# Kernel tuning notes

Measured on AMD Instinct MI355X. Metric: run time of the kernel, lower is better.

Reference implementation:

```python
import jax, jax.numpy as jnp
import numpy as np

N = 100000      # nodes
E = 1600000     # edges (avg degree 16)
F_IN = 64       # num_features
HID = 16        # hidden channels (fixed in module)
OUT = 32        # num_classes
K = 2           # kernel_size (dim=1, degree=1 open B-spline -> 2 basis fns)


def setup_inputs() -> dict:
    key = jax.random.key(0)
    ks = jax.random.split(key, 8)
    return {
        "x": jax.random.normal(ks[0], (N, F_IN), jnp.float32),
        "edge_index": jax.random.randint(ks[1], (2, E), 0, N, dtype=jnp.int64),
        "dropout": 0,  # unused in eval mode (F.dropout training=False)
        "edge_attr": jnp.full((E, 1), 0.1, jnp.float32),  # nt([0.1]) broadcast per edge
        "W1": jax.random.normal(ks[2], (K, F_IN, HID), jnp.float32) / np.sqrt(K * F_IN).astype(np.float32),
        "root1": jax.random.normal(ks[3], (F_IN, HID), jnp.float32) / np.sqrt(F_IN).astype(np.float32),
        "bias1": jnp.zeros((HID,), jnp.float32),
        "W2": jax.random.normal(ks[4], (K, HID, OUT), jnp.float32) / np.sqrt(K * HID).astype(np.float32),
        "root2": jax.random.normal(ks[5], (HID, OUT), jnp.float32) / np.sqrt(HID).astype(np.float32),
        "bias2": jnp.zeros((OUT,), jnp.float32),
    }


def spline_conv(x, edge_index, edge_attr, W, root, bias):
    """SplineConv, dim=1, kernel_size=2, degree=1 open B-spline, aggr='mean'."""
    src, dst = edge_index[0], edge_index[1]
    n = x.shape[0]
    u = edge_attr[:, 0]                                  # [E] pseudo-coords in [0,1]
    # degree-1 open spline, kernel_size=2: frac = u*(ks-1) = u; kernels {0,1}
    basis = jnp.stack([1.0 - u, u], axis=1)              # [E, K]
    # transform at node level (cheaper than gathering raw features per edge)
    h = jnp.einsum('nf,kfo->nko', x, W)                  # [N, K, out]
    msg = jnp.einsum('ek,eko->eo', basis, h[src])        # [E, out]
    summed = jax.ops.segment_sum(msg, dst, num_segments=n)
    deg = jax.ops.segment_sum(jnp.ones_like(u), dst, num_segments=n)
    out = summed / jnp.maximum(deg, 1.0)[:, None]        # mean aggregation
    return out + x @ root + bias                          # root weight + bias


def reference(x, edge_index, dropout, edge_attr, W1, root1, bias1, W2, root2, bias2):
    # dropout is a no-op in eval mode
    h = jax.nn.elu(spline_conv(x, edge_index, edge_attr, W1, root1, bias1))
    h = spline_conv(h, edge_index, edge_attr, W2, root2, bias2)
    return jax.nn.log_softmax(h, axis=1)
```

## Files before the change

### kernel.cpp

```cpp
#include <hip/hip_runtime.h>
#include <math.h>

#define NN 100000
#define NE 1600000
#define F_IN 64
#define HID 16
#define OUTF 32
#define BKT_SHIFT 6
#define BKT_NODES 64
#define NBKT 1563
#define SRCM 0x1FFFF
#define CAP_REG 2048
#define CAP_LDS 1184
#define PBLK2 1000
#define EPB2 1600
#define OVF_MAX 4096

__device__ __forceinline__ unsigned bf16r(float f) {
    unsigned u = __float_as_uint(f);
    return (u + 0x7FFFu + ((u >> 16) & 1u)) >> 16;
}
__device__ __forceinline__ float bfa(unsigned p) { return __uint_as_float(p << 16); }
__device__ __forceinline__ float bfd(unsigned p) { return __uint_as_float(p & 0xFFFF0000u); }
__device__ __forceinline__ float bfh(unsigned short v) { return __uint_as_float(((unsigned)v) << 16); }

__device__ __forceinline__ void acc8(uint4 hv, float u, float* s0, float* s1) {
    unsigned w[4] = {hv.x, hv.y, hv.z, hv.w};
#pragma unroll
    for (int q = 0; q < 4; ++q) {
        float lo = __uint_as_float(w[q] << 16);
        float hi = __uint_as_float(w[q] & 0xFFFF0000u);
        s0[2 * q]     += lo; s1[2 * q]     = fmaf(u, lo, s1[2 * q]);
        s0[2 * q + 1] += hi; s1[2 * q + 1] = fmaf(u, hi, s1[2 * q + 1]);
    }
}
__device__ __forceinline__ void acc4(uint4 ap, float u, float* a) {
    unsigned w[4] = {ap.x, ap.y, ap.z, ap.w};
#pragma unroll
    for (int q = 0; q < 4; ++q)
        a[q] += fmaf(u, bfd(w[q]), bfa(w[q]));
}

__global__ __launch_bounds__(1024) void partF_kernel(const int* __restrict__ ei,
                                                     const float* __restrict__ ea,
                                                     int* __restrict__ gcur,
                                                     int* __restrict__ novf,
                                                     int4* __restrict__ ovf,
                                                     int2* __restrict__ bkt) {
    __shared__ int hcnt[NBKT];
    __shared__ int cur[NBKT];
    __shared__ int lbase[NBKT + 1];
    __shared__ int pw[16];
    __shared__ int2 sbuf[EPB2];
    int t = threadIdx.x, blk = blockIdx.x;
    for (int i = t; i < NBKT; i += 1024) { hcnt[i] = 0; cur[i] = 0; }
    __syncthreads();
    int beg = blk * EPB2;
    int4 d4 = make_int4(0, 0, 0, 0);
    bool act = (4 * t) < EPB2;
    if (act) {
        d4 = *(const int4*)(ei + NE + beg + 4 * t);
        atomicAdd(&hcnt[d4.x >> BKT_SHIFT], 1);
        atomicAdd(&hcnt[d4.y >> BKT_SHIFT], 1);
        atomicAdd(&hcnt[d4.z >> BKT_SHIFT], 1);
        atomicAdd(&hcnt[d4.w >> BKT_SHIFT], 1);
    }
    __syncthreads();
    int i0 = 2 * t, i1 = 2 * t + 1;
    int v0 = (i0 < NBKT) ? hcnt[i0] : 0;
    int v1 = (i1 < NBKT) ? hcnt[i1] : 0;
    int ts = v0 + v1;
    int lane = t & 63, wid = t >> 6;
    int sc = ts;
#pragma unroll
    for (int off = 1; off < 64; off <<= 1) {
        int o = __shfl_up(sc, off, 64);
        if (lane >= off) sc += o;
    }
    if (lane == 63) pw[wid] = sc;
    __syncthreads();
    if (t < 16) {
        int p = pw[t];
        int q = p;
#pragma unroll
        for (int off = 1; off < 16; off <<= 1) {
            int o = __shfl_up(q, off, 64);
            if (t >= off) q += o;
        }
        pw[t] = q - p;
    }
    __syncthreads();
    int ebase = pw[wid] + (sc - ts);
    if (i0 < NBKT) lbase[i0] = ebase;
    if (i1 < NBKT) lbase[i1] = ebase + v0;
    if (t == 0) lbase[NBKT] = EPB2;
    __syncthreads();
    int rot = (blk * 397) % NBKT;
    for (int k = t; k < NBKT; k += 1024) {
        int i = k + rot; if (i >= NBKT) i -= NBKT;
        int c = hcnt[i];
        hcnt[i] = c ? (atomicAdd(&gcur[i], c) - lbase[i]) : 0;
    }
    __syncthreads();
    if (act) {
        int4 s4 = *(const int4*)(ei + beg + 4 * t);
        float4 u4 = *(const float4*)(ea + beg + 4 * t);
        int dst[4] = {d4.x, d4.y, d4.z, d4.w};
        int src[4] = {s4.x, s4.y, s4.z, s4.w};
        float uu[4] = {u4.x, u4.y, u4.z, u4.w};
#pragma unroll
        for (int k = 0; k < 4; ++k) {
            int b = dst[k] >> BKT_SHIFT;
            int r = atomicAdd(&cur[b], 1);
            sbuf[lbase[b] + r] = make_int2(src[k] | ((dst[k] & (BKT_NODES - 1)) << 17),
                                           __float_as_int(uu[k]));
        }
    }
    __syncthreads();
    for (int i = t; i < EPB2; i += 1024) {
        int lo = 0, hi = NBKT - 1;
        while (lo < hi) {
            int mid = (lo + hi + 1) >> 1;
            if (lbase[mid] <= i) lo = mid; else hi = mid - 1;
        }
        int b = lo;
        int2 pk = sbuf[i];
        int p = hcnt[b] + i;
        if (p < CAP_REG) {
            bkt[(size_t)b * CAP_REG + p] = pk;
        } else {
            int o = atomicAdd(novf, 1);
            if (o < OVF_MAX)
                ovf[o] = make_int4(b * BKT_NODES + (((unsigned)pk.x) >> 17), pk.x & SRCM, pk.y, 0);
        }
    }
}

__global__ __launch_bounds__(256) void proj1z_kernel(const float* __restrict__ x,
                                                     const float* __restrict__ W1,
                                                     const float* __restrict__ root1,
                                                     const float* __restrict__ bias1,
                                                     unsigned* __restrict__ ab1p,
                                                     float* __restrict__ r1,
                                                     int* __restrict__ gcur,
                                                     int* __restrict__ novf) {
    int gz = blockIdx.x * 256 + threadIdx.x;
    if (gz < NBKT) gcur[gz] = 0;
    if (gz == NBKT) novf[0] = 0;
    __shared__ float w[2 * F_IN * HID];
    __shared__ float wr[F_IN * HID];
    __shared__ float bb[HID];
    for (int i = threadIdx.x; i < 2 * F_IN * HID; i += 256) w[i] = W1[i];
    for (int i = threadIdx.x; i < F_IN * HID; i += 256) wr[i] = root1[i];
    if (threadIdx.x < HID) bb[threadIdx.x] = bias1[threadIdx.x];
    __syncthreads();
    int n = blockIdx.x * 256 + threadIdx.x;
    if (n >= NN) return;
    float accA[HID], accB[HID], accR[HID];
#pragma unroll
    for (int o = 0; o < HID; ++o) { accA[o] = 0.f; accB[o] = 0.f; accR[o] = bb[o]; }
    const float4* xr4 = (const float4*)(x + (size_t)n * F_IN);
    for (int f4 = 0; f4 < F_IN / 4; ++f4) {
        float4 xv4 = xr4[f4];
        float xs[4] = {xv4.x, xv4.y, xv4.z, xv4.w};
#pragma unroll
        for (int q = 0; q < 4; ++q) {
            int f = f4 * 4 + q;
            float xv = xs[q];
            const float* w0 = &w[f * HID];
            const float* w1 = &w[F_IN * HID + f * HID];
            const float* w2 = &wr[f * HID];
#pragma unroll
            for (int o = 0; o < HID; ++o) {
                accA[o] = fmaf(xv, w0[o], accA[o]);
                accB[o] = fmaf(xv, w1[o], accB[o]);
                accR[o] = fmaf(xv, w2[o], accR[o]);
            }
        }
    }
    unsigned* ar = ab1p + (size_t)n * HID;
    float* rr = r1 + (size_t)n * HID;
#pragma unroll
    for (int o = 0; o < HID; ++o) {
        ar[o] = bf16r(accA[o]) | (bf16r(accB[o] - accA[o]) << 16);
        rr[o] = accR[o];
    }
}

__global__ __launch_bounds__(256) void gather1_kernel(const int* __restrict__ gcur,
                                                      const int* __restrict__ novf,
                                                      const int4* __restrict__ ovf,
                                                      int2* __restrict__ bkt,
                                                      const unsigned* __restrict__ ab1p,
                                                      const float* __restrict__ r1,
                                                      unsigned short* __restrict__ h16,
                                                      float* __restrict__ dinv,
                                                      int* __restrict__ segg) {
    __shared__ int2 sorted[CAP_LDS];
    __shared__ int cnt[BKT_NODES], cur[BKT_NODES], segb[BKT_NODES + 1];
    __shared__ float degsL[BKT_NODES];
    int t = threadIdx.x;
    int b = blockIdx.x;
    int tot = gcur[b];
    int beg = b * CAP_REG;
    if (t < BKT_NODES) { cnt[t] = 0; cur[t] = 0; degsL[t] = 0.f; }
    __syncthreads();
    int nodeBase = b * BKT_NODES;

    if (tot <= CAP_LDS) {
        for (int e = t; e < tot; e += 256)
            atomicAdd(&cnt[((unsigned)bkt[beg + e].x) >> 17], 1);
        __syncthreads();
        if (t < BKT_NODES) {
            int v = cnt[t];
            int sc = v;
#pragma unroll
            for (int off = 1; off < 64; off <<= 1) {
                int o = __shfl_up(sc, off, 64);
                if (t >= off) sc += o;
            }
            segb[t] = sc - v;
            if (t == 63) segb[64] = sc;
        }
        __syncthreads();
        for (int e = t; e < tot; e += 256) {
            int2 pk = bkt[beg + e];
            int loc = ((unsigned)pk.x) >> 17;
            int pos = segb[loc] + atomicAdd(&cur[loc], 1);
            sorted[pos] = pk;
        }
        __syncthreads();
        int nv = tot >> 1;
        int4* s4 = (int4*)sorted;
        int4* o4 = (int4*)(bkt + beg);
        for (int i = t; i < nv; i += 256) o4[i] = s4[i];
        if (t == 0 && (tot & 1)) bkt[beg + tot - 1] = sorted[tot - 1];
        if (t <= BKT_NODES) segg[b * (BKT_NODES + 1) + t] = segb[t];
        int node = t >> 2;
        int jq = t & 3;
        int s0 = segb[node], e2 = segb[node + 1];
        float acc[4] = {0.f, 0.f, 0.f, 0.f};
        int e = s0;
        for (; e + 3 < e2; e += 4) {
            int2 p0 = sorted[e];
            int2 p1 = sorted[e + 1];
            int2 p2 = sorted[e + 2];
            int2 p3 = sorted[e + 3];
            uint4 a0 = *(const uint4*)(ab1p + ((size_t)(p0.x & SRCM) << 4) + (jq << 2));
            uint4 a1 = *(const uint4*)(ab1p + ((size_t)(p1.x & SRCM) << 4) + (jq << 2));
            uint4 a2 = *(const uint4*)(ab1p + ((size_t)(p2.x & SRCM) << 4) + (jq << 2));
            uint4 a3 = *(const uint4*)(ab1p + ((size_t)(p3.x & SRCM) << 4) + (jq << 2));
            acc4(a0, __int_as_float(p0.y), acc);
            acc4(a1, __int_as_float(p1.y), acc);
            acc4(a2, __int_as_float(p2.y), acc);
            acc4(a3, __int_as_float(p3.y), acc);
        }
        for (; e < e2; ++e) {
            int2 pk = sorted[e];
            uint4 ap = *(const uint4*)(ab1p + ((size_t)(pk.x & SRCM) << 4) + (jq << 2));
            acc4(ap, __int_as_float(pk.y), acc);
        }
        int n = nodeBase + node;
        if (n < NN) {
            float d0 = 1.f / (float)max(e2 - s0, 1);
            float4 rv = *(const float4*)(r1 + ((size_t)n << 4) + (jq << 2));
            float rr[4] = {rv.x, rv.y, rv.z, rv.w};
            unsigned hw[4];
#pragma unroll
            for (int k = 0; k < 4; ++k) {
                float v = acc[k] * d0 + rr[k];
                hw[k] = bf16r(v > 0.f ? v : expm1f(v));
            }
            *(uint2*)(h16 + ((size_t)n << 4) + (jq << 2)) =
                make_uint2(hw[0] | (hw[1] << 16), hw[2] | (hw[3] << 16));
            if (jq == 0) dinv[n] = d0;
        }
    } else {
        float* accL = (float*)sorted;
        int inreg = min(tot, CAP_REG);
        int end = beg + inreg;
        for (int i = t; i < BKT_NODES * HID; i += 256) accL[i] = 0.f;
        __syncthreads();
        int j = t & (HID - 1);
        int g = t >> 4;
        for (int e = beg + g; e < end; e += 16) {
            int2 pk = bkt[e];
            unsigned p = ab1p[(size_t)(pk.x & SRCM) * HID + j];
            atomicAdd(&accL[(((unsigned)pk.x) >> 17) * HID + j],
                      fmaf(__int_as_float(pk.y), bfd(p), bfa(p)));
            if (j == 0) atomicAdd(&degsL[((unsigned)pk.x) >> 17], 1.f);
        }
        int ovn = min(novf[0], OVF_MAX);
        for (int o = 0; o < ovn; ++o) {
            int4 ent = ovf[o];
            int loc = ent.x - nodeBase;
            if (loc >= 0 && loc < BKT_NODES && g == 0) {
                unsigned p = ab1p[(size_t)ent.y * HID + j];
                atomicAdd(&accL[loc * HID + j], fmaf(__int_as_float(ent.z), bfd(p), bfa(p)));
                if (j == 0) atomicAdd(&degsL[loc], 1.f);
            }
        }
        __syncthreads();
        if (t < BKT_NODES) degsL[t] = 1.f / fmaxf(degsL[t], 1.f);
        if (t == 0) segg[b * (BKT_NODES + 1)] = -1;
        __syncthreads();
        for (int idx = t; idx < BKT_NODES * HID; idx += 256) {
            int nl = idx >> 4, jj = idx & (HID - 1);
            int n = nodeBase + nl;
            if (n < NN) {
                float v = accL[idx] * degsL[nl] + r1[(size_t)n * HID + jj];
                h16[(size_t)n * HID + jj] = (unsigned short)bf16r(v > 0.f ? v : expm1f(v));
            }
        }
        if (t < BKT_NODES && nodeBase + t < NN) dinv[nodeBase + t] = degsL[t];
    }
}

#define HB_NODES 32
__global__ __launch_bounds__(256) void gather2_kernel(const int* __restrict__ gcur,
                                                      const int* __restrict__ novf,
                                                      const int4* __restrict__ ovf,
                                                      const int2* __restrict__ bkt,
                                                      const unsigned short* __restrict__ h16,
                                                      const float* __restrict__ W2,
                                                      const float* __restrict__ root2,
                                                      const float* __restrict__ bias2,
                                                      const float* __restrict__ dinv,
                                                      const int* __restrict__ segg,
                                                      float* __restrict__ out) {
    __shared__ float w20[HID * OUTF], w2d[HID * OUTF], wr[HID * OUTF];
    __shared__ float bb[OUTF];
    __shared__ int segb[HB_NODES + 1];
    __shared__ int sflag;
    int t = threadIdx.x;
    int b2 = blockIdx.x;
    int b = b2 >> 1;
    int h = b2 & 1;
    for (int i = t; i < HID * OUTF; i += 256) {
        float a = W2[i];
        w20[i] = a;
        w2d[i] = W2[HID * OUTF + i] - a;
        wr[i] = root2[i];
    }
    if (t < OUTF) bb[t] = bias2[t];
    int tot = gcur[b];
    int beg = b * CAP_REG;
    int nodeBase = b * BKT_NODES + h * HB_NODES;
    if (t <= HB_NODES) segb[t] = segg[b * (BKT_NODES + 1) + h * HB_NODES + t];
    if (t == 0) sflag = segg[b * (BKT_NODES + 1)];
    __syncthreads();

    int node = t >> 3;
    int li = t & 7;
    int sub = li >> 1;
    int jh = li & 1;
    float S0[8] = {0.f, 0.f, 0.f, 0.f, 0.f, 0.f, 0.f, 0.f};
    float S1[8] = {0.f, 0.f, 0.f, 0.f, 0.f, 0.f, 0.f, 0.f};

    if (tot <= CAP_LDS && sflag != -1) {
        const int2* sp = bkt + beg;
        int s = segb[node], e2 = segb[node + 1];
        int e = s + sub;
        for (; e + 12 < e2; e += 16) {
            int2 p0 = sp[e];
            int2 p1 = sp[e + 4];
            int2 p2 = sp[e + 8];
            int2 p3 = sp[e + 12];
            uint4 h0 = *(const uint4*)(h16 + ((size_t)(p0.x & SRCM) << 4) + (jh << 3));
            uint4 h1 = *(const uint4*)(h16 + ((size_t)(p1.x & SRCM) << 4) + (jh << 3));
            uint4 h2 = *(const uint4*)(h16 + ((size_t)(p2.x & SRCM) << 4) + (jh << 3));
            uint4 h3 = *(const uint4*)(h16 + ((size_t)(p3.x & SRCM) << 4) + (jh << 3));
            acc8(h0, __int_as_float(p0.y), S0, S1);
            acc8(h1, __int_as_float(p1.y), S0, S1);
            acc8(h2, __int_as_float(p2.y), S0, S1);
            acc8(h3, __int_as_float(p3.y), S0, S1);
        }
        for (; e < e2; e += 4) {
            int2 pk = sp[e];
            uint4 hv = *(const uint4*)(h16 + ((size_t)(pk.x & SRCM) << 4) + (jh << 3));
            acc8(hv, __int_as_float(pk.y), S0, S1);
        }
#pragma unroll
        for (int k = 0; k < 8; ++k) {
            S0[k] += __shfl_xor(S0[k], 2); S0[k] += __shfl_xor(S0[k], 4);
            S1[k] += __shfl_xor(S1[k], 2); S1[k] += __shfl_xor(S1[k], 4);
        }
    } else {
        float* s0L = w20;
        float* s1L = w2d;
        for (int i = t; i < HB_NODES * HID; i += 256) { s0L[i] = 0.f; s1L[i] = 0.f; }
        __syncthreads();
        int j = t & (HID - 1);
        int g = t >> 4;
        int inreg = min(tot, CAP_REG);
        int end = beg + inreg;
        for (int e = beg + g; e < end; e += 16) {
            int2 pk = bkt[e];
            int loc = ((unsigned)pk.x) >> 17;
            if ((loc >> 5) == h) {
                float hvv = bfh(h16[(size_t)(pk.x & SRCM) * HID + j]);
                atomicAdd(&s0L[(loc & 31) * HID + j], hvv);
                atomicAdd(&s1L[(loc & 31) * HID + j], __int_as_float(pk.y) * hvv);
            }
        }
        int ovn = min(novf[0], OVF_MAX);
        for (int o = 0; o < ovn; ++o) {
            int4 ent = ovf[o];
            int loc = ent.x - nodeBase;
            if (loc >= 0 && loc < HB_NODES && g == 0) {
                float hvv = bfh(h16[(size_t)ent.y * HID + j]);
                atomicAdd(&s0L[loc * HID + j], hvv);
                atomicAdd(&s1L[loc * HID + j], __int_as_float(ent.z) * hvv);
            }
        }
        __syncthreads();
#pragma unroll
        for (int k = 0; k < 8; ++k) {
            S0[k] = s0L[node * HID + jh * 8 + k];
            S1[k] = s1L[node * HID + jh * 8 + k];
        }
        __syncthreads();
        for (int i = t; i < HID * OUTF; i += 256) {
            float a = W2[i];
            w20[i] = a;
            w2d[i] = W2[HID * OUTF + i] - a;
        }
        __syncthreads();
    }

    float F0[16], F1[16];
#pragma unroll
    for (int k = 0; k < 8; ++k) {
        float p0 = __shfl_xor(S0[k], 1);
        float p1 = __shfl_xor(S1[k], 1);
        F0[k] = jh ? p0 : S0[k];
        F0[8 + k] = jh ? S0[k] : p0;
        F1[k] = jh ? p1 : S1[k];
        F1[8 + k] = jh ? S1[k] : p1;
    }
    int n = nodeBase + node;
    if (n < NN) {
        float di = dinv[n];
        uint4 hA = *(const uint4*)(h16 + ((size_t)n << 4));
        uint4 hB = *(const uint4*)(h16 + ((size_t)n << 4) + 8);
        float hf[16];
        unsigned wa[4] = {hA.x, hA.y, hA.z, hA.w};
        unsigned wb[4] = {hB.x, hB.y, hB.z, hB.w};
#pragma unroll
        for (int q = 0; q < 4; ++q) {
            hf[2 * q]     = __uint_as_float(wa[q] << 16);
            hf[2 * q + 1] = __uint_as_float(wa[q] & 0xFFFF0000u);
            hf[8 + 2 * q]     = __uint_as_float(wb[q] << 16);
            hf[8 + 2 * q + 1] = __uint_as_float(wb[q] & 0xFFFF0000u);
        }
        float outv[4];
#pragma unroll
        for (int q = 0; q < 4; ++q) {
            int jj = li * 4 + q;
            float ms = 0.f;
#pragma unroll
            for (int f = 0; f < HID; ++f)
                ms += F0[f] * w20[f * OUTF + jj] + F1[f] * w2d[f * OUTF + jj];
            float v = ms * di + bb[jj];
#pragma unroll
            for (int f = 0; f < HID; ++f)
                v = fmaf(hf[f], wr[f * OUTF + jj], v);
            outv[q] = v;
        }
        float m = fmaxf(fmaxf(outv[0], outv[1]), fmaxf(outv[2], outv[3]));
        m = fmaxf(m, __shfl_xor(m, 1));
        m = fmaxf(m, __shfl_xor(m, 2));
        m = fmaxf(m, __shfl_xor(m, 4));
        float sl = expf(outv[0] - m) + expf(outv[1] - m) + expf(outv[2] - m) + expf(outv[3] - m);
        sl += __shfl_xor(sl, 1);
        sl += __shfl_xor(sl, 2);
        sl += __shfl_xor(sl, 4);
        float lse = m + logf(sl);
        *(float4*)(out + (size_t)n * OUTF + li * 4) =
            make_float4(outv[0] - lse, outv[1] - lse, outv[2] - lse, outv[3] - lse);
    }
}

extern "C" void kernel_launch(void* const* d_in, const int* in_sizes, int n_in,
                              void* d_out, int out_size, void* d_ws, size_t ws_size,
                              hipStream_t stream) {
    const float* x     = (const float*)d_in[0];
    const int*   ei    = (const int*)d_in[1];
    const float* ea    = (const float*)d_in[3];
    const float* W1    = (const float*)d_in[4];
    const float* root1 = (const float*)d_in[5];
    const float* bias1 = (const float*)d_in[6];
    const float* W2    = (const float*)d_in[7];
    const float* root2 = (const float*)d_in[8];
    const float* bias2 = (const float*)d_in[9];
    float* out = (float*)d_out;
    float* ws  = (float*)d_ws;

    const size_t N = NN;
    int*            gcur = (int*)(ws);
    int*            novf = (int*)(ws + 2000);
    int4*           ovf  = (int4*)(ws + 2048);
    float*          dinv = ws + 20000;
    int*            segg = (int*)(ws + 120000);
    float*          r1   = ws + 222000;
    unsigned*       ab1p = (unsigned*)(ws + 222000 + 16 * N);
    unsigned short* h16  = (unsigned short*)(ws + 222000 + 32 * N);
    int2*           bkt  = (int2*)(ws + 222000 + 40 * N);

    int nbN = (NN + 255) / 256;
    proj1z_kernel<<<nbN, 256, 0, stream>>>(x, W1, root1, bias1, ab1p, r1, gcur, novf);
    partF_kernel<<<PBLK2, 1024, 0, stream>>>(ei, ea, gcur, novf, ovf, bkt);
    gather1_kernel<<<NBKT, 256, 0, stream>>>(gcur, novf, ovf, bkt, ab1p, r1, h16, dinv, segg);
    gather2_kernel<<<NBKT * 2, 256, 0, stream>>>(gcur, novf, ovf, bkt, h16, W2, root2, bias2, dinv, segg, out);
}
```

Measured before the change: 119.1 us.

## Partition edges with fewer blocks processing multiple chunks each

The edge-bucketing kernel now runs 200 blocks, each handling 8000 edges in four 2000-edge chunks, instead of 1000 blocks of 1600 edges. Each block counts its whole range once and reserves global bucket space with one atomic per bucket. It then sorts each chunk locally in LDS and writes it out, advancing per-bucket positions as it goes. The aim is fewer global atomics on the bucket cursors and longer contiguous runs per bucket. The cost is fewer blocks to fill the GPU, destination indices read twice per chunk, and many more barriers per block.

```diff
diff --git a/kernel.cpp b/kernel.cpp
--- a/kernel.cpp
+++ b/kernel.cpp
@@ -12,8 +12,10 @@
 #define SRCM 0x1FFFF
 #define CAP_REG 2048
 #define CAP_LDS 1184
-#define PBLK2 1000
-#define EPB2 1600
+#define PBLK3 200
+#define EPB3 8000
+#define CHUNK 2000
+#define NCHK 4
 #define OVF_MAX 4096
 
 __device__ __forceinline__ unsigned bf16r(float f) {
@@ -47,92 +49,109 @@
                                                      int* __restrict__ novf,
                                                      int4* __restrict__ ovf,
                                                      int2* __restrict__ bkt) {
-    __shared__ int hcnt[NBKT];
-    __shared__ int cur[NBKT];
-    __shared__ int lbase[NBKT + 1];
+    __shared__ int gpos[NBKT];
+    __shared__ int segc[NBKT];
     __shared__ int pw[16];
-    __shared__ int2 sbuf[EPB2];
+    __shared__ int2 sbuf[CHUNK];
     int t = threadIdx.x, blk = blockIdx.x;
-    for (int i = t; i < NBKT; i += 1024) { hcnt[i] = 0; cur[i] = 0; }
+    for (int i = t; i < NBKT; i += 1024) gpos[i] = 0;
     __syncthreads();
-    int beg = blk * EPB2;
-    int4 d4 = make_int4(0, 0, 0, 0);
-    bool act = (4 * t) < EPB2;
-    if (act) {
-        d4 = *(const int4*)(ei + NE + beg + 4 * t);
-        atomicAdd(&hcnt[d4.x >> BKT_SHIFT], 1);
-        atomicAdd(&hcnt[d4.y >> BKT_SHIFT], 1);
-        atomicAdd(&hcnt[d4.z >> BKT_SHIFT], 1);
-        atomicAdd(&hcnt[d4.w >> BKT_SHIFT], 1);
-    }
-    __syncthreads();
-    int i0 = 2 * t, i1 = 2 * t + 1;
-    int v0 = (i0 < NBKT) ? hcnt[i0] : 0;
-    int v1 = (i1 < NBKT) ? hcnt[i1] : 0;
-    int ts = v0 + v1;
-    int lane = t & 63, wid = t >> 6;
-    int sc = ts;
-#pragma unroll
-    for (int off = 1; off < 64; off <<= 1) {
-        int o = __shfl_up(sc, off, 64);
-        if (lane >= off) sc += o;
-    }
-    if (lane == 63) pw[wid] = sc;
-    __syncthreads();
-    if (t < 16) {
-        int p = pw[t];
-        int q = p;
-#pragma unroll
-        for (int off = 1; off < 16; off <<= 1) {
-            int o = __shfl_up(q, off, 64);
-            if (t >= off) q += o;
-        }
-        pw[t] = q - p;
-    }
-    __syncthreads();
-    int ebase = pw[wid] + (sc - ts);
-    if (i0 < NBKT) lbase[i0] = ebase;
-    if (i1 < NBKT) lbase[i1] = ebase + v0;
-    if (t == 0) lbase[NBKT] = EPB2;
+    int beg = blk * EPB3;
+    for (int i = t; i < EPB3 / 4; i += 1024) {
+        int4 d4 = *(const int4*)(ei + NE + beg + 4 * i);
+        atomicAdd(&gpos[d4.x >> BKT_SHIFT], 1);
+        atomicAdd(&gpos[d4.y >> BKT_SHIFT], 1);
+        atomicAdd(&gpos[d4.z >> BKT_SHIFT], 1);
+        atomicAdd(&gpos[d4.w >> BKT_SHIFT], 1);
+    }
     __syncthreads();
     int rot = (blk * 397) % NBKT;
     for (int k = t; k < NBKT; k += 1024) {
         int i = k + rot; if (i >= NBKT) i -= NBKT;
-        int c = hcnt[i];
-        hcnt[i] = c ? (atomicAdd(&gcur[i], c) - lbase[i]) : 0;
+        int c = gpos[i];
+        gpos[i] = c ? atomicAdd(&gcur[i], c) : 0;
     }
     __syncthreads();
-    if (act) {
-        int4 s4 = *(const int4*)(ei + beg + 4 * t);
-        float4 u4 = *(const float4*)(ea + beg + 4 * t);
-        int dst[4] = {d4.x, d4.y, d4.z, d4.w};
-        int src[4] = {s4.x, s4.y, s4.z, s4.w};
-        float uu[4] = {u4.x, u4.y, u4.z, u4.w};
-#pragma unroll
-        for (int k = 0; k < 4; ++k) {
-            int b = dst[k] >> BKT_SHIFT;
-            int r = atomicAdd(&cur[b], 1);
-            sbuf[lbase[b] + r] = make_int2(src[k] | ((dst[k] & (BKT_NODES - 1)) << 17),
-                                           __float_as_int(uu[k]));
-        }
-    }
-    __syncthreads();
-    for (int i = t; i < EPB2; i += 1024) {
-        int lo = 0, hi = NBKT - 1;
-        while (lo < hi) {
-            int mid = (lo + hi + 1) >> 1;
-            if (lbase[mid] <= i) lo = mid; else hi = mid - 1;
-        }
-        int b = lo;
-        int2 pk = sbuf[i];
-        int p = hcnt[b] + i;
-        if (p < CAP_REG) {
-            bkt[(size_t)b * CAP_REG + p] = pk;
-        } else {
-            int o = atomicAdd(novf, 1);
-            if (o < OVF_MAX)
-                ovf[o] = make_int4(b * BKT_NODES + (((unsigned)pk.x) >> 17), pk.x & SRCM, pk.y, 0);
-        }
+    for (int c = 0; c < NCHK; ++c) {
+        int cbeg = beg + c * CHUNK;
+        for (int i = t; i < NBKT; i += 1024) segc[i] = 0;
+        __syncthreads();
+        for (int i = t; i < CHUNK / 4; i += 1024) {
+            int4 d4 = *(const int4*)(ei + NE + cbeg + 4 * i);
+            atomicAdd(&segc[d4.x >> BKT_SHIFT], 1);
+            atomicAdd(&segc[d4.y >> BKT_SHIFT], 1);
+            atomicAdd(&segc[d4.z >> BKT_SHIFT], 1);
+            atomicAdd(&segc[d4.w >> BKT_SHIFT], 1);
+        }
+        __syncthreads();
+        int i0 = 2 * t, i1 = 2 * t + 1;
+        int v0 = (i0 < NBKT) ? segc[i0] : 0;
+        int v1 = (i1 < NBKT) ? segc[i1] : 0;
+        int ts = v0 + v1;
+        int lane = t & 63, wid = t >> 6;
+        int sc = ts;
+#pragma unroll
+        for (int off = 1; off < 64; off <<= 1) {
+            int o = __shfl_up(sc, off, 64);
+            if (lane >= off) sc += o;
+        }
+        if (lane == 63) pw[wid] = sc;
+        __syncthreads();
+        if (t < 16) {
+            int p = pw[t];
+            int q = p;
+#pragma unroll
+            for (int off = 1; off < 16; off <<= 1) {
+                int o = __shfl_up(q, off, 64);
+                if (t >= off) q += o;
+            }
+            pw[t] = q - p;
+        }
+        __syncthreads();
+        int ebase = pw[wid] + (sc - ts);
+        if (i0 < NBKT) segc[i0] = ebase;
+        if (i1 < NBKT) segc[i1] = ebase + v0;
+        __syncthreads();
+        for (int i = t; i < CHUNK / 4; i += 1024) {
+            int4 d4 = *(const int4*)(ei + NE + cbeg + 4 * i);
+            int4 s4 = *(const int4*)(ei + cbeg + 4 * i);
+            float4 u4 = *(const float4*)(ea + cbeg + 4 * i);
+            int dst[4] = {d4.x, d4.y, d4.z, d4.w};
+            int src[4] = {s4.x, s4.y, s4.z, s4.w};
+            float uu[4] = {u4.x, u4.y, u4.z, u4.w};
+#pragma unroll
+            for (int k = 0; k < 4; ++k) {
+                int b = dst[k] >> BKT_SHIFT;
+                int pos = atomicAdd(&segc[b], 1);
+                sbuf[pos] = make_int2(src[k] | ((dst[k] & (BKT_NODES - 1)) << 17),
+                                      __float_as_int(uu[k]));
+            }
+        }
+        __syncthreads();
+        for (int i = t; i < CHUNK; i += 1024) {
+            int lo = 0, hi = NBKT - 1;
+            while (lo < hi) {
+                int mid = (lo + hi) >> 1;
+                if (segc[mid] > i) hi = mid; else lo = mid + 1;
+            }
+            int b = lo;
+            int start = b ? segc[b - 1] : 0;
+            int p = gpos[b] + (i - start);
+            int2 pk = sbuf[i];
+            if (p < CAP_REG) {
+                bkt[(size_t)b * CAP_REG + p] = pk;
+            } else {
+                int o = atomicAdd(novf, 1);
+                if (o < OVF_MAX)
+                    ovf[o] = make_int4(b * BKT_NODES + (((unsigned)pk.x) >> 17), pk.x & SRCM, pk.y, 0);
+            }
+        }
+        __syncthreads();
+        for (int b = t; b < NBKT; b += 1024) {
+            int start = b ? segc[b - 1] : 0;
+            gpos[b] += segc[b] - start;
+        }
+        __syncthreads();
     }
 }
 
@@ -509,7 +528,7 @@
 
     int nbN = (NN + 255) / 256;
     proj1z_kernel<<<nbN, 256, 0, stream>>>(x, W1, root1, bias1, ab1p, r1, gcur, novf);
-    partF_kernel<<<PBLK2, 1024, 0, stream>>>(ei, ea, gcur, novf, ovf, bkt);
+    partF_kernel<<<PBLK3, 1024, 0, stream>>>(ei, ea, gcur, novf, ovf, bkt);
     gather1_kernel<<<NBKT, 256, 0, stream>>>(gcur, novf, ovf, bkt, ab1p, r1, h16, dinv, segg);
     gather2_kernel<<<NBKT * 2, 256, 0, stream>>>(gcur, novf, ovf, bkt, h16, W2, root2, bias2, dinv, segg, out);
 }
```

Result: faster. 112.1 us (-5.9%).
